# Kernel optimization log

Hardware: AMD Instinct MI355X
Metric: run time of the kernel (lower is better)

Reference implementation:

```python
import jax, jax.numpy as jnp
import numpy as np

NEG_INF = -1.0e9
LN_EPS = 1e-5
LEAK = 0.2


def setup_inputs() -> dict:
    key = jax.random.key(0)
    ks = jax.random.split(key, 8)
    B, C, T, N, H = 8, 64, 24, 512, 2
    hd = C // H
    x = jax.random.normal(ks[0], (B, C, T, N), dtype=jnp.float32)
    gso = jax.random.randint(ks[1], (N, N), 0, 2, dtype=jnp.int32)
    # torch nn.Linear weights are (out, in); xavier-ish scale
    s = (2.0 / (C + C)) ** 0.5
    Wq = jax.random.normal(ks[2], (C, C), dtype=jnp.float32) * s
    Wk = jax.random.normal(ks[3], (C, C), dtype=jnp.float32) * s
    Wv = jax.random.normal(ks[4], (C, C), dtype=jnp.float32) * s
    sa = (2.0 / (H + hd)) ** 0.5
    a_src = jax.random.normal(ks[5], (H, hd), dtype=jnp.float32) * sa
    a_dst = jax.random.normal(ks[6], (H, hd), dtype=jnp.float32) * sa
    ln_gamma = jnp.ones((C,), dtype=jnp.float32)
    ln_beta = jnp.zeros((C,), dtype=jnp.float32)
    return {"x": x, "gso": gso, "Wq": Wq, "Wk": Wk, "Wv": Wv,
            "a_src": a_src, "a_dst": a_dst, "ln_gamma": ln_gamma, "ln_beta": ln_beta}


def _spatial_gat(x, gso, Wq, Wk, Wv, a_src, a_dst, ln_gamma, ln_beta):
    B, C, T, N = x.shape
    H, hd = a_src.shape
    # (B, C, T, N) -> (B*T, N, C)
    xr = jnp.transpose(x, (0, 2, 3, 1)).reshape(B * T, N, C)
    # torch Linear: y = x @ W.T
    Q = jnp.einsum('bnc,dc->bnd', xr, Wq).reshape(B * T, N, H, hd)
    K = jnp.einsum('bnc,dc->bnd', xr, Wk).reshape(B * T, N, H, hd)
    V = jnp.einsum('bnc,dc->bnd', xr, Wv).reshape(B * T, N, H, hd)
    # additive GAT scores, all heads at once
    s_src = jnp.einsum('bnhd,hd->bnh', Q, a_src)  # (BT, N, H)
    s_dst = jnp.einsum('bnhd,hd->bnh', K, a_dst)  # (BT, N, H)
    scores = jax.nn.leaky_relu(s_src[:, :, None, :] + s_dst[:, None, :, :], LEAK)  # (BT, Ni, Nj, H)
    mask = jnp.where(gso == 0, jnp.float32(NEG_INF), jnp.float32(0.0))  # (N, N)
    scores = scores + mask[None, :, :, None]
    attn = jax.nn.softmax(scores, axis=2)  # softmax over destination j
    out = jnp.einsum('bijh,bjhd->bihd', attn, V)  # (BT, N, H, hd)
    out = out.reshape(B * T, N, C)
    # LayerNorm over channel dim
    mu = jnp.mean(out, axis=-1, keepdims=True)
    var = jnp.var(out, axis=-1, keepdims=True)
    out = (out - mu) * jax.lax.rsqrt(var + LN_EPS) * ln_gamma + ln_beta
    # back to (B, C, T, N)
    return jnp.transpose(out.reshape(B, T, N, C), (0, 3, 1, 2))


def reference(x, gso, Wq, Wk, Wv, a_src, a_dst, ln_gamma, ln_beta):
    return _spatial_gat(x, gso, Wq, Wk, Wv, a_src, a_dst, ln_gamma, ln_beta)
```

## Files before the change

### kernel.cpp

```cpp
#include <hip/hip_runtime.h>

#define CDIM 64
#define TDIM 24
#define NDIM 512
#define NBT  192

typedef float    float4v __attribute__((ext_vector_type(4)));
typedef _Float16 half8v  __attribute__((ext_vector_type(8)));
typedef _Float16 half4v  __attribute__((ext_vector_type(4)));
typedef _Float16 half2v  __attribute__((ext_vector_type(2)));


__device__ __forceinline__ float exp2_fast(float x) {
#if __has_builtin(__builtin_amdgcn_exp2f)
  return __builtin_amdgcn_exp2f(x);
#else
  return __expf(x * 0.69314718f);
#endif
}

__device__ __forceinline__ half2v pk2(float a, float b) {
  return __builtin_bit_cast(half2v, __builtin_amdgcn_cvt_pkrtz(a, b));
}

struct SmemK1 {
  union {
    _Float16 xt[128][72];
    _Float16 vtb[64][136];
  } big;
  _Float16 wv[64][72];
  _Float16 wext[16][72];
};

__launch_bounds__(256, 4)
__global__ void k1_v(const float* __restrict__ x,  const float* __restrict__ Wv,
                     const float* __restrict__ Wq, const float* __restrict__ Wk,
                     const float* __restrict__ a_src, const float* __restrict__ a_dst,
                     const int* __restrict__ gso,
                     _Float16* __restrict__ VT_g,
                     float* __restrict__ s_src_g, float* __restrict__ s_dst_g,
                     unsigned char* __restrict__ maskb) {
  const int t  = threadIdx.x;
  const int bx = blockIdx.x;

  if (bx >= 768) {
    int g = (bx - 768) * 256 + t;
    const int4* gp = (const int4*)gso + (size_t)g * 4;
    unsigned w[4];
#pragma unroll
    for (int k = 0; k < 4; ++k) {
      int4 v = gp[k];
      w[k] = (v.x ? 0x000000FFu : 0u) | (v.y ? 0x0000FF00u : 0u) |
             (v.z ? 0x00FF0000u : 0u) | (v.w ? 0xFF000000u : 0u);
    }
    uint4 o; o.x = w[0]; o.y = w[1]; o.z = w[2]; o.w = w[3];
    ((uint4*)maskb)[g] = o;
    return;
  }

  __shared__ SmemK1 sm;
  const int bt = bx % NBT;
  const int qn = bx / NBT;
  const int b  = bt / TDIM, tt = bt % TDIM;
  const int n0 = qn * 128;

#pragma unroll
  for (int it = 0; it < 4; ++it) {
    int idx = it * 256 + t;
    int d = idx >> 4, k4 = (idx & 15) * 4;
    float4 v = ((const float4*)Wv)[idx];
    half2v p0 = pk2(v.x, v.y), p1 = pk2(v.z, v.w);
    half4v h4; h4[0] = p0[0]; h4[1] = p0[1]; h4[2] = p1[0]; h4[3] = p1[1];
    *(half4v*)&sm.wv[d][k4] = h4;
  }
  for (int z = t; z < 12 * 72; z += 256) ((_Float16*)sm.wext[4])[z] = (_Float16)0.f;
  {
    int r = t >> 6, c = t & 63;
    const float* av = (r & 2) ? a_dst : a_src;
    const float* W  = (r & 2) ? Wk : Wq;
    int off = (r & 1) * 32;
    float s = 0.f;
#pragma unroll
    for (int d = 0; d < 32; ++d)
      s += av[off + d] * W[(off + d) * 64 + c];
    sm.wext[r][c] = (_Float16)(s * 1.44269504f);
  }
  for (int it = 0; it < 16; ++it) {
    int idx = it * 256 + t;
    int cp = idx >> 7, n = idx & 127;
    int c0 = cp * 2;
    const float* base = x + ((size_t)(b * CDIM + c0) * TDIM + tt) * NDIM + n0 + n;
    *(half2v*)&sm.big.xt[n][c0] = pk2(base[0], base[(size_t)TDIM * NDIM]);
  }
  __syncthreads();

  const int lane = t & 63, w = t >> 6;
  const int m = lane & 15, quad = lane >> 4;
  const int mbase = w * 32;

  float4v acc[2][5];
#pragma unroll
  for (int mt = 0; mt < 2; ++mt)
#pragma unroll
    for (int nt = 0; nt < 5; ++nt)
#pragma unroll
      for (int r = 0; r < 4; ++r) acc[mt][nt][r] = 0.f;

#pragma unroll
  for (int ks = 0; ks < 2; ++ks) {
    half8v af[2], bf[5];
#pragma unroll
    for (int mt = 0; mt < 2; ++mt)
      af[mt] = *(const half8v*)&sm.big.xt[mbase + mt * 16 + m][ks * 32 + quad * 8];
#pragma unroll
    for (int nt = 0; nt < 4; ++nt)
      bf[nt] = *(const half8v*)&sm.wv[nt * 16 + m][ks * 32 + quad * 8];
    bf[4] = *(const half8v*)&sm.wext[m][ks * 32 + quad * 8];
#pragma unroll
    for (int mt = 0; mt < 2; ++mt)
#pragma unroll
      for (int nt = 0; nt < 5; ++nt)
        acc[mt][nt] = __builtin_amdgcn_mfma_f32_16x16x32_f16(af[mt], bf[nt], acc[mt][nt], 0, 0, 0);
  }

  if (m < 4) {
    float* basep = (m < 2 ? s_src_g : s_dst_g) + (size_t)(bt * 2 + (m & 1)) * NDIM;
#pragma unroll
    for (int mt = 0; mt < 2; ++mt)
#pragma unroll
      for (int r = 0; r < 4; ++r)
        basep[n0 + mbase + mt * 16 + quad * 4 + r] = acc[mt][4][r];
  }
  __syncthreads();

#pragma unroll
  for (int mt = 0; mt < 2; ++mt)
#pragma unroll
    for (int nt = 0; nt < 4; ++nt)
#pragma unroll
      for (int r = 0; r < 4; r += 2) {
        int nl = mbase + mt * 16 + quad * 4 + r;
        int c  = nt * 16 + m;
        *(half2v*)&sm.big.vtb[c][nl] = pk2(acc[mt][nt][r], acc[mt][nt][r + 1]);
      }
  __syncthreads();

  const unsigned* vdw = (const unsigned*)sm.big.vtb;
  unsigned* outdw = (unsigned*)VT_g;
  for (int it = 0; it < 16; ++it) {
    int idx = it * 256 + t;
    int c = idx >> 6, jd = idx & 63;
    outdw[(size_t)(bt * 64 + c) * 256 + qn * 64 + jd] = vdw[c * 68 + jd];
  }
}

struct SmemK2 {
  union {
    _Float16 vt[64][128];
    float otile[64][66];
  } u;
  union {
    struct { _Float16 F[2][512]; _Float16 P[2][512]; } f;
    struct { float rsum[4][64]; float rsq[4][64]; float mu[64]; float rs[64]; } l;
  } v;
};

__launch_bounds__(256, 6)
__global__ void k2_attn(const _Float16* __restrict__ VT_g,
                        const float* __restrict__ s_src_g, const float* __restrict__ s_dst_g,
                        const unsigned char* __restrict__ maskb,
                        const float* __restrict__ gamma, const float* __restrict__ beta,
                        float* __restrict__ out) {
  __shared__ SmemK2 sm;
  const int t     = threadIdx.x;
  const int bx    = blockIdx.x;
  const int bt    = bx % NBT;
  const int itile = bx / NBT;
  const int i0    = itile * 64;
  const int b     = bt / TDIM, tt = bt % TDIM;
  const int lane  = t & 63, w = t >> 6;
  const int h = w >> 1, ihalf = w & 1;
  const int m = lane & 15, quad = lane >> 4;

  for (int it = 0; it < 4; ++it) {
    int idx = it * 256 + t;
    float d = s_dst_g[(size_t)bt * 2 * NDIM + idx];
    ((_Float16*)sm.v.f.F)[idx] = (_Float16)exp2_fast(d);
    ((_Float16*)sm.v.f.P)[idx] = (_Float16)exp2_fast(0.2f * d);
  }
  half8v E8[2], Q8[2];
#pragma unroll
  for (int mt = 0; mt < 2; ++mt) {
    float sv = s_src_g[(size_t)(bt * 2 + h) * NDIM + i0 + ihalf * 32 + mt * 16 + m];
    _Float16 ev = (_Float16)exp2_fast(sv - 6.f);
    _Float16 qv = (_Float16)exp2_fast(0.2f * sv - 6.f);
#pragma unroll
    for (int jj = 0; jj < 8; ++jj) { E8[mt][jj] = ev; Q8[mt][jj] = qv; }
  }

  float4v acc[2][2], accs[2];
#pragma unroll
  for (int mt = 0; mt < 2; ++mt) {
#pragma unroll
    for (int r = 0; r < 4; ++r) { acc[mt][0][r] = 0.f; acc[mt][1][r] = 0.f; accs[mt][r] = 0.f; }
  }
  const half8v bones = {(_Float16)1.f, (_Float16)1.f, (_Float16)1.f, (_Float16)1.f,
                        (_Float16)1.f, (_Float16)1.f, (_Float16)1.f, (_Float16)1.f};

  const unsigned char* mrow0 = maskb + (size_t)(i0 + ihalf * 32 + m) * NDIM;
  const unsigned char* mrow1 = mrow0 + 16 * NDIM;
  const uint4* vsrc = (const uint4*)VT_g + (size_t)bt * 64 * 64;
  const int r0 = h * 32 + m;
  const int rsw = (r0 & 7) * 8;

  for (int js = 0; js < 4; ++js) {
    __syncthreads();
#pragma unroll
    for (int it = 0; it < 4; ++it) {
      int idx = it * 256 + t;
      int c = idx >> 4, ch = idx & 15;
      uint4 val = vsrc[c * 64 + js * 16 + ch];
      *(uint4*)&sm.u.vt[c][(ch * 8) ^ ((c & 7) * 8)] = val;
    }
    __syncthreads();

#pragma unroll
    for (int ksl = 0; ksl < 4; ++ksl) {
      int jq = ksl * 32 + quad * 8;
      int jo = js * 128 + jq;
      half8v F8 = *(const half8v*)&sm.v.f.F[h][jo];
      half8v P8 = *(const half8v*)&sm.v.f.P[h][jo];
      half8v b0 = *(const half8v*)&sm.u.vt[r0][jq ^ rsw];
      half8v b1 = *(const half8v*)&sm.u.vt[r0 + 16][jq ^ rsw];
      uint2 mv0 = *(const uint2*)(mrow0 + jo);
      uint2 mv1 = *(const uint2*)(mrow1 + jo);
#pragma unroll
      for (int mt = 0; mt < 2; ++mt) {
        uint2 mv = mt ? mv1 : mv0;
        half8v e8 = __builtin_elementwise_max(E8[mt] * F8, Q8[mt] * P8);
        uint4 eu = __builtin_bit_cast(uint4, e8);
        eu.x &= __builtin_amdgcn_perm(0u, mv.x, 0x01010000u);
        eu.y &= __builtin_amdgcn_perm(0u, mv.x, 0x03030202u);
        eu.z &= __builtin_amdgcn_perm(0u, mv.y, 0x01010000u);
        eu.w &= __builtin_amdgcn_perm(0u, mv.y, 0x03030202u);
        half8v af = __builtin_bit_cast(half8v, eu);
        acc[mt][0] = __builtin_amdgcn_mfma_f32_16x16x32_f16(af, b0,    acc[mt][0], 0, 0, 0);
        acc[mt][1] = __builtin_amdgcn_mfma_f32_16x16x32_f16(af, b1,    acc[mt][1], 0, 0, 0);
        accs[mt]   = __builtin_amdgcn_mfma_f32_16x16x32_f16(af, bones, accs[mt],   0, 0, 0);
      }
    }
  }

  __syncthreads();
#pragma unroll
  for (int mt = 0; mt < 2; ++mt)
#pragma unroll
    for (int r = 0; r < 4; ++r) {
      float sc = __builtin_amdgcn_rcpf(accs[mt][r]);
      int i_loc = ihalf * 32 + mt * 16 + quad * 4 + r;
#pragma unroll
      for (int nt = 0; nt < 2; ++nt)
        sm.u.otile[i_loc][h * 32 + nt * 16 + m] = acc[mt][nt][r] * sc;
    }
  __syncthreads();

  {
    int i = t & 63, cg = t >> 6;
    float s1 = 0.f, s2 = 0.f;
#pragma unroll
    for (int cc = 0; cc < 16; ++cc) {
      float v = sm.u.otile[i][cg * 16 + cc];
      s1 += v; s2 += v * v;
    }
    sm.v.l.rsum[cg][i] = s1;
    sm.v.l.rsq[cg][i]  = s2;
  }
  __syncthreads();
  if (t < 64) {
    int i = t;
    float s1 = 0.f, s2 = 0.f;
#pragma unroll
    for (int cg = 0; cg < 4; ++cg) { s1 += sm.v.l.rsum[cg][i]; s2 += sm.v.l.rsq[cg][i]; }
    float mu  = s1 * (1.f / 64.f);
    float var = s2 * (1.f / 64.f) - mu * mu;
    sm.v.l.mu[i] = mu;
    sm.v.l.rs[i] = rsqrtf(var + 1e-5f);
  }
  __syncthreads();
  {
    int i = t & 63, cg = t >> 6;
    float mu = sm.v.l.mu[i], rs = sm.v.l.rs[i];
    int n = i0 + i;
#pragma unroll
    for (int cc = 0; cc < 16; ++cc) {
      int c = cg * 16 + cc;
      float v = (sm.u.otile[i][c] - mu) * rs * gamma[c] + beta[c];
      out[((size_t)(b * CDIM + c) * TDIM + tt) * NDIM + n] = v;
    }
  }
}

extern "C" void kernel_launch(void* const* d_in, const int* in_sizes, int n_in,
                              void* d_out, int out_size, void* d_ws, size_t ws_size,
                              hipStream_t stream) {
  const float* x     = (const float*)d_in[0];
  const int*   gso   = (const int*)d_in[1];
  const float* Wq    = (const float*)d_in[2];
  const float* Wk    = (const float*)d_in[3];
  const float* Wv    = (const float*)d_in[4];
  const float* a_src = (const float*)d_in[5];
  const float* a_dst = (const float*)d_in[6];
  const float* gamma = (const float*)d_in[7];
  const float* beta  = (const float*)d_in[8];
  float* out = (float*)d_out;

  char* ws = (char*)d_ws;
  _Float16* VT_g  = (_Float16*)ws;
  float*    s_src = (float*)(ws + 12582912);
  float*    s_dst = (float*)(ws + 13369344);
  unsigned char* maskb = (unsigned char*)(ws + 14155776);

  k1_v<<<832, 256, 0, stream>>>(x, Wv, Wq, Wk, a_src, a_dst, gso,
                                VT_g, s_src, s_dst, maskb);
  k2_attn<<<1536, 256, 0, stream>>>(VT_g, s_src, s_dst, maskb, gamma, beta, out);
}
```

Before: 133.2 us.

## Double-buffer V tiles in LDS and register-prefetch next tile and mask

The attention kernel now loads the next V^T slab and mask bytes into registers while the current slab is consumed, writing into one of two LDS buffers so only one barrier per iteration is needed. This aims to hide global load latency behind the MFMA loop. In exchange LDS use doubles and register pressure rises, so the occupancy hint drops from 6 to 4 blocks per CU.

```diff
diff --git a/kernel.cpp b/kernel.cpp
--- a/kernel.cpp
+++ b/kernel.cpp
@@ -156,7 +156,7 @@
 
 struct SmemK2 {
   union {
-    _Float16 vt[64][128];
+    _Float16 vt[2][64][128];
     float otile[64][66];
   } u;
   union {
@@ -165,7 +165,7 @@
   } v;
 };
 
-__launch_bounds__(256, 6)
+__launch_bounds__(256, 4)
 __global__ void k2_attn(const _Float16* __restrict__ VT_g,
                         const float* __restrict__ s_src_g, const float* __restrict__ s_dst_g,
                         const unsigned char* __restrict__ maskb,
@@ -182,6 +182,25 @@
   const int h = w >> 1, ihalf = w & 1;
   const int m = lane & 15, quad = lane >> 4;
 
+  const unsigned char* mrow0 = maskb + (size_t)(i0 + ihalf * 32 + m) * NDIM;
+  const unsigned char* mrow1 = mrow0 + 16 * NDIM;
+  const uint4* vsrc = (const uint4*)VT_g + (size_t)bt * 64 * 64;
+  const int r0 = h * 32 + m;
+  const int rsw = (r0 & 7) * 8;
+  const int sc = t >> 4, sch = t & 15;
+
+  uint4 pre[4];
+#pragma unroll
+  for (int it = 0; it < 4; ++it)
+    pre[it] = vsrc[(sc + it * 16) * 64 + sch];
+  uint2 mpre0[4], mpre1[4];
+#pragma unroll
+  for (int k = 0; k < 4; ++k) {
+    int jo = k * 32 + quad * 8;
+    mpre0[k] = *(const uint2*)(mrow0 + jo);
+    mpre1[k] = *(const uint2*)(mrow1 + jo);
+  }
+
   for (int it = 0; it < 4; ++it) {
     int idx = it * 256 + t;
     float d = s_dst_g[(size_t)bt * 2 * NDIM + idx];
@@ -207,36 +226,41 @@
   const half8v bones = {(_Float16)1.f, (_Float16)1.f, (_Float16)1.f, (_Float16)1.f,
                         (_Float16)1.f, (_Float16)1.f, (_Float16)1.f, (_Float16)1.f};
 
-  const unsigned char* mrow0 = maskb + (size_t)(i0 + ihalf * 32 + m) * NDIM;
-  const unsigned char* mrow1 = mrow0 + 16 * NDIM;
-  const uint4* vsrc = (const uint4*)VT_g + (size_t)bt * 64 * 64;
-  const int r0 = h * 32 + m;
-  const int rsw = (r0 & 7) * 8;
-
   for (int js = 0; js < 4; ++js) {
+    uint4 nxt[4]; uint2 mn0[4], mn1[4];
+    if (js < 3) {
+#pragma unroll
+      for (int it = 0; it < 4; ++it)
+        nxt[it] = vsrc[(sc + it * 16) * 64 + (js + 1) * 16 + sch];
+#pragma unroll
+      for (int k = 0; k < 4; ++k) {
+        int jo = (js + 1) * 128 + k * 32 + quad * 8;
+        mn0[k] = *(const uint2*)(mrow0 + jo);
+        mn1[k] = *(const uint2*)(mrow1 + jo);
+      }
+    }
+    {
+      _Float16* vbuf = &sm.u.vt[js & 1][0][0];
+#pragma unroll
+      for (int it = 0; it < 4; ++it) {
+        int c = sc + it * 16;
+        *(uint4*)&vbuf[c * 128 + ((sch * 8) ^ ((c & 7) * 8))] = pre[it];
+      }
+    }
     __syncthreads();
-#pragma unroll
-    for (int it = 0; it < 4; ++it) {
-      int idx = it * 256 + t;
-      int c = idx >> 4, ch = idx & 15;
-      uint4 val = vsrc[c * 64 + js * 16 + ch];
-      *(uint4*)&sm.u.vt[c][(ch * 8) ^ ((c & 7) * 8)] = val;
-    }
-    __syncthreads();
-
+
+    const _Float16* vb = &sm.u.vt[js & 1][0][0];
 #pragma unroll
     for (int ksl = 0; ksl < 4; ++ksl) {
       int jq = ksl * 32 + quad * 8;
       int jo = js * 128 + jq;
       half8v F8 = *(const half8v*)&sm.v.f.F[h][jo];
       half8v P8 = *(const half8v*)&sm.v.f.P[h][jo];
-      half8v b0 = *(const half8v*)&sm.u.vt[r0][jq ^ rsw];
-      half8v b1 = *(const half8v*)&sm.u.vt[r0 + 16][jq ^ rsw];
-      uint2 mv0 = *(const uint2*)(mrow0 + jo);
-      uint2 mv1 = *(const uint2*)(mrow1 + jo);
+      half8v b0 = *(const half8v*)&vb[r0 * 128 + (jq ^ rsw)];
+      half8v b1 = *(const half8v*)&vb[(r0 + 16) * 128 + (jq ^ rsw)];
 #pragma unroll
       for (int mt = 0; mt < 2; ++mt) {
-        uint2 mv = mt ? mv1 : mv0;
+        uint2 mv = mt ? mpre1[ksl] : mpre0[ksl];
         half8v e8 = __builtin_elementwise_max(E8[mt] * F8, Q8[mt] * P8);
         uint4 eu = __builtin_bit_cast(uint4, e8);
         eu.x &= __builtin_amdgcn_perm(0u, mv.x, 0x01010000u);
@@ -249,6 +273,10 @@
         accs[mt]   = __builtin_amdgcn_mfma_f32_16x16x32_f16(af, bones, accs[mt],   0, 0, 0);
       }
     }
+#pragma unroll
+    for (int it = 0; it < 4; ++it) pre[it] = nxt[it];
+#pragma unroll
+    for (int k = 0; k < 4; ++k) { mpre0[k] = mn0[k]; mpre1[k] = mn1[k]; }
   }
 
   __syncthreads();
@@ -256,11 +284,11 @@
   for (int mt = 0; mt < 2; ++mt)
 #pragma unroll
     for (int r = 0; r < 4; ++r) {
-      float sc = __builtin_amdgcn_rcpf(accs[mt][r]);
+      float sc2 = __builtin_amdgcn_rcpf(accs[mt][r]);
       int i_loc = ihalf * 32 + mt * 16 + quad * 4 + r;
 #pragma unroll
       for (int nt = 0; nt < 2; ++nt)
-        sm.u.otile[i_loc][h * 32 + nt * 16 + m] = acc[mt][nt][r] * sc;
+        sm.u.otile[i_loc][h * 32 + nt * 16 + m] = acc[mt][nt][r] * sc2;
     }
   __syncthreads();
 
```

Measured after the change: 175.2 us. +31.5%, slower.

## Double the attention i-tile and stream V/mask from global with 3-stage register prefetch

Applied to the files above, without the earlier changes.

The attention kernel now handles 128 query rows per block instead of 64, so each V fragment loaded is reused across four row tiles instead of two. The staging of V through shared memory with its barriers is replaced by direct global loads into registers, prefetched two steps ahead through a three-slot ring. The aim is to halve V traffic per output and remove synchronisation from the main loop. In exchange it uses more registers (launch bounds drop to 2 blocks), a larger shared output tile, and half as many blocks.

```diff
diff --git a/kernel.cpp b/kernel.cpp
--- a/kernel.cpp
+++ b/kernel.cpp
@@ -156,31 +156,47 @@
 
 struct SmemK2 {
   union {
-    _Float16 vt[64][128];
-    float otile[64][66];
-  } u;
-  union {
     struct { _Float16 F[2][512]; _Float16 P[2][512]; } f;
-    struct { float rsum[4][64]; float rsq[4][64]; float mu[64]; float rs[64]; } l;
+    struct { float rsum[2][128]; float rsq[2][128];
+             float mu[128]; float rs[128]; } l;
   } v;
+  float otile[128][66];
 };
 
-__launch_bounds__(256, 6)
+__launch_bounds__(256, 2)
 __global__ void k2_attn(const _Float16* __restrict__ VT_g,
                         const float* __restrict__ s_src_g, const float* __restrict__ s_dst_g,
                         const unsigned char* __restrict__ maskb,
                         const float* __restrict__ gamma, const float* __restrict__ beta,
                         float* __restrict__ out) {
   __shared__ SmemK2 sm;
-  const int t     = threadIdx.x;
-  const int bx    = blockIdx.x;
-  const int bt    = bx % NBT;
-  const int itile = bx / NBT;
-  const int i0    = itile * 64;
-  const int b     = bt / TDIM, tt = bt % TDIM;
-  const int lane  = t & 63, w = t >> 6;
+  const int t    = threadIdx.x;
+  const int bx   = blockIdx.x;
+  const int bt   = bx % NBT;
+  const int ip   = bx / NBT;
+  const int i0   = ip * 128;
+  const int b    = bt / TDIM, tt = bt % TDIM;
+  const int lane = t & 63, w = t >> 6;
   const int h = w >> 1, ihalf = w & 1;
   const int m = lane & 15, quad = lane >> 4;
+
+  const _Float16* vrow = VT_g + ((size_t)bt * 64 + h * 32 + m) * NDIM;
+  const unsigned char* mrow[4];
+  mrow[0] = maskb + (size_t)(i0 + ihalf * 32 + m) * NDIM;
+  mrow[1] = mrow[0] + 16 * NDIM;
+  mrow[2] = mrow[0] + 64 * NDIM;
+  mrow[3] = mrow[0] + 80 * NDIM;
+
+  half8v pv0[3], pv1[3];
+  uint2  pm[3][4];
+#pragma unroll
+  for (int k = 0; k < 2; ++k) {
+    int jo = k * 32 + quad * 8;
+    pv0[k] = *(const half8v*)(vrow + jo);
+    pv1[k] = *(const half8v*)(vrow + 16 * NDIM + jo);
+#pragma unroll
+    for (int mt = 0; mt < 4; ++mt) pm[k][mt] = *(const uint2*)(mrow[mt] + jo);
+  }
 
   for (int it = 0; it < 4; ++it) {
     int idx = it * 256 + t;
@@ -188,99 +204,85 @@
     ((_Float16*)sm.v.f.F)[idx] = (_Float16)exp2_fast(d);
     ((_Float16*)sm.v.f.P)[idx] = (_Float16)exp2_fast(0.2f * d);
   }
-  half8v E8[2], Q8[2];
-#pragma unroll
-  for (int mt = 0; mt < 2; ++mt) {
-    float sv = s_src_g[(size_t)(bt * 2 + h) * NDIM + i0 + ihalf * 32 + mt * 16 + m];
+  half8v E8[4], Q8[4];
+#pragma unroll
+  for (int mt = 0; mt < 4; ++mt) {
+    int irow = i0 + (mt >> 1) * 64 + ihalf * 32 + (mt & 1) * 16 + m;
+    float sv = s_src_g[(size_t)(bt * 2 + h) * NDIM + irow];
     _Float16 ev = (_Float16)exp2_fast(sv - 6.f);
     _Float16 qv = (_Float16)exp2_fast(0.2f * sv - 6.f);
 #pragma unroll
     for (int jj = 0; jj < 8; ++jj) { E8[mt][jj] = ev; Q8[mt][jj] = qv; }
   }
 
-  float4v acc[2][2], accs[2];
-#pragma unroll
-  for (int mt = 0; mt < 2; ++mt) {
+  float4v acc[4][2], accs[4];
+#pragma unroll
+  for (int mt = 0; mt < 4; ++mt)
 #pragma unroll
     for (int r = 0; r < 4; ++r) { acc[mt][0][r] = 0.f; acc[mt][1][r] = 0.f; accs[mt][r] = 0.f; }
-  }
   const half8v bones = {(_Float16)1.f, (_Float16)1.f, (_Float16)1.f, (_Float16)1.f,
                         (_Float16)1.f, (_Float16)1.f, (_Float16)1.f, (_Float16)1.f};
 
-  const unsigned char* mrow0 = maskb + (size_t)(i0 + ihalf * 32 + m) * NDIM;
-  const unsigned char* mrow1 = mrow0 + 16 * NDIM;
-  const uint4* vsrc = (const uint4*)VT_g + (size_t)bt * 64 * 64;
-  const int r0 = h * 32 + m;
-  const int rsw = (r0 & 7) * 8;
-
-  for (int js = 0; js < 4; ++js) {
-    __syncthreads();
-#pragma unroll
-    for (int it = 0; it < 4; ++it) {
-      int idx = it * 256 + t;
-      int c = idx >> 4, ch = idx & 15;
-      uint4 val = vsrc[c * 64 + js * 16 + ch];
-      *(uint4*)&sm.u.vt[c][(ch * 8) ^ ((c & 7) * 8)] = val;
-    }
-    __syncthreads();
-
-#pragma unroll
-    for (int ksl = 0; ksl < 4; ++ksl) {
-      int jq = ksl * 32 + quad * 8;
-      int jo = js * 128 + jq;
-      half8v F8 = *(const half8v*)&sm.v.f.F[h][jo];
-      half8v P8 = *(const half8v*)&sm.v.f.P[h][jo];
-      half8v b0 = *(const half8v*)&sm.u.vt[r0][jq ^ rsw];
-      half8v b1 = *(const half8v*)&sm.u.vt[r0 + 16][jq ^ rsw];
-      uint2 mv0 = *(const uint2*)(mrow0 + jo);
-      uint2 mv1 = *(const uint2*)(mrow1 + jo);
-#pragma unroll
-      for (int mt = 0; mt < 2; ++mt) {
-        uint2 mv = mt ? mv1 : mv0;
-        half8v e8 = __builtin_elementwise_max(E8[mt] * F8, Q8[mt] * P8);
-        uint4 eu = __builtin_bit_cast(uint4, e8);
-        eu.x &= __builtin_amdgcn_perm(0u, mv.x, 0x01010000u);
-        eu.y &= __builtin_amdgcn_perm(0u, mv.x, 0x03030202u);
-        eu.z &= __builtin_amdgcn_perm(0u, mv.y, 0x01010000u);
-        eu.w &= __builtin_amdgcn_perm(0u, mv.y, 0x03030202u);
-        half8v af = __builtin_bit_cast(half8v, eu);
-        acc[mt][0] = __builtin_amdgcn_mfma_f32_16x16x32_f16(af, b0,    acc[mt][0], 0, 0, 0);
-        acc[mt][1] = __builtin_amdgcn_mfma_f32_16x16x32_f16(af, b1,    acc[mt][1], 0, 0, 0);
-        accs[mt]   = __builtin_amdgcn_mfma_f32_16x16x32_f16(af, bones, accs[mt],   0, 0, 0);
-      }
-    }
-  }
-
-  __syncthreads();
-#pragma unroll
-  for (int mt = 0; mt < 2; ++mt)
+  __syncthreads();
+
+#pragma unroll
+  for (int it = 0; it < 16; ++it) {
+    const int s = it % 3;
+    if (it < 14) {
+      const int f = (it + 2) % 3;
+      const int jo = (it + 2) * 32 + quad * 8;
+      pv0[f] = *(const half8v*)(vrow + jo);
+      pv1[f] = *(const half8v*)(vrow + 16 * NDIM + jo);
+#pragma unroll
+      for (int mt = 0; mt < 4; ++mt) pm[f][mt] = *(const uint2*)(mrow[mt] + jo);
+    }
+    const int jo = it * 32 + quad * 8;
+    half8v F8 = *(const half8v*)&sm.v.f.F[h][jo];
+    half8v P8 = *(const half8v*)&sm.v.f.P[h][jo];
+#pragma unroll
+    for (int mt = 0; mt < 4; ++mt) {
+      half8v e8 = __builtin_elementwise_max(E8[mt] * F8, Q8[mt] * P8);
+      uint4 eu = __builtin_bit_cast(uint4, e8);
+      uint2 mv = pm[s][mt];
+      eu.x &= __builtin_amdgcn_perm(0u, mv.x, 0x01010000u);
+      eu.y &= __builtin_amdgcn_perm(0u, mv.x, 0x03030202u);
+      eu.z &= __builtin_amdgcn_perm(0u, mv.y, 0x01010000u);
+      eu.w &= __builtin_amdgcn_perm(0u, mv.y, 0x03030202u);
+      half8v af = __builtin_bit_cast(half8v, eu);
+      acc[mt][0] = __builtin_amdgcn_mfma_f32_16x16x32_f16(af, pv0[s], acc[mt][0], 0, 0, 0);
+      acc[mt][1] = __builtin_amdgcn_mfma_f32_16x16x32_f16(af, pv1[s], acc[mt][1], 0, 0, 0);
+      accs[mt]   = __builtin_amdgcn_mfma_f32_16x16x32_f16(af, bones,  accs[mt],   0, 0, 0);
+    }
+  }
+
+#pragma unroll
+  for (int mt = 0; mt < 4; ++mt)
 #pragma unroll
     for (int r = 0; r < 4; ++r) {
       float sc = __builtin_amdgcn_rcpf(accs[mt][r]);
-      int i_loc = ihalf * 32 + mt * 16 + quad * 4 + r;
+      int i_loc = (mt >> 1) * 64 + ihalf * 32 + (mt & 1) * 16 + quad * 4 + r;
 #pragma unroll
       for (int nt = 0; nt < 2; ++nt)
-        sm.u.otile[i_loc][h * 32 + nt * 16 + m] = acc[mt][nt][r] * sc;
+        sm.otile[i_loc][h * 32 + nt * 16 + m] = acc[mt][nt][r] * sc;
     }
   __syncthreads();
 
   {
-    int i = t & 63, cg = t >> 6;
+    int i = t & 127, cg = t >> 7;
     float s1 = 0.f, s2 = 0.f;
 #pragma unroll
-    for (int cc = 0; cc < 16; ++cc) {
-      float v = sm.u.otile[i][cg * 16 + cc];
+    for (int cc = 0; cc < 32; ++cc) {
+      float v = sm.otile[i][cg * 32 + cc];
       s1 += v; s2 += v * v;
     }
     sm.v.l.rsum[cg][i] = s1;
     sm.v.l.rsq[cg][i]  = s2;
   }
   __syncthreads();
-  if (t < 64) {
+  if (t < 128) {
     int i = t;
-    float s1 = 0.f, s2 = 0.f;
-#pragma unroll
-    for (int cg = 0; cg < 4; ++cg) { s1 += sm.v.l.rsum[cg][i]; s2 += sm.v.l.rsq[cg][i]; }
+    float s1 = sm.v.l.rsum[0][i] + sm.v.l.rsum[1][i];
+    float s2 = sm.v.l.rsq[0][i]  + sm.v.l.rsq[1][i];
     float mu  = s1 * (1.f / 64.f);
     float var = s2 * (1.f / 64.f) - mu * mu;
     sm.v.l.mu[i] = mu;
@@ -288,13 +290,13 @@
   }
   __syncthreads();
   {
-    int i = t & 63, cg = t >> 6;
+    int i = t & 127, cg = t >> 7;
     float mu = sm.v.l.mu[i], rs = sm.v.l.rs[i];
     int n = i0 + i;
 #pragma unroll
-    for (int cc = 0; cc < 16; ++cc) {
-      int c = cg * 16 + cc;
-      float v = (sm.u.otile[i][c] - mu) * rs * gamma[c] + beta[c];
+    for (int cc = 0; cc < 32; ++cc) {
+      int c = cg * 32 + cc;
+      float v = (sm.otile[i][c] - mu) * rs * gamma[c] + beta[c];
       out[((size_t)(b * CDIM + c) * TDIM + tt) * NDIM + n] = v;
     }
   }
@@ -322,5 +324,5 @@
 
   k1_v<<<832, 256, 0, stream>>>(x, Wv, Wq, Wk, a_src, a_dst, gso,
                                 VT_g, s_src, s_dst, maskb);
-  k2_attn<<<1536, 256, 0, stream>>>(VT_g, s_src, s_dst, maskb, gamma, beta, out);
-}
+  k2_attn<<<768, 256, 0, stream>>>(VT_g, s_src, s_dst, maskb, gamma, beta, out);
+}
```

After: 130.8 us. Within noise of the previous version (-1.8%).
